# Kernel optimization log

Hardware: AMD Instinct MI355X
Metric: run time of the kernel (lower is better)

Reference implementation:

```python
import jax, jax.numpy as jnp
import numpy as np

N = 100000
E = 3200000
H = 128
ED = 16
P = 6  # 2**(sample_hop+1)-2 with sample_hop=2


def setup_inputs() -> dict:
    key = jax.random.key(0)
    ks = jax.random.split(key, 8)
    q = jax.random.normal(ks[0], (N, H), jnp.float32)
    k = jax.random.normal(ks[1], (N, H), jnp.float32)
    v = jax.random.normal(ks[2], (N, H), jnp.float32)
    eigs = jax.random.normal(ks[3], (N, ED), jnp.float32)
    lambda0 = jnp.zeros((1,), jnp.float32)
    path_emb_w = jax.random.normal(ks[4], (P, 1), jnp.float32)
    indices = jax.random.randint(ks[5], (2, E), 0, N, dtype=jnp.int32)
    path_type = jax.random.randint(ks[6], (E,), 0, P, dtype=jnp.int32)
    return {"q": q, "k": k, "v": v, "eigs": eigs, "lambda0": lambda0,
            "path_emb_w": path_emb_w, "indices": indices, "path_type": path_type}


def _segment_softmax(vals, seg, num_segments):
    # numerically stable softmax over edges grouped by destination row `seg`
    m = jax.ops.segment_max(vals, seg, num_segments=num_segments)
    m = jnp.where(jnp.isfinite(m), m, 0.0)  # empty segments -> 0, harmless
    e = jnp.exp(vals - m[seg])
    d = jax.ops.segment_sum(e, seg, num_segments=num_segments)
    return e / d[seg]


def reference(q, k, v, eigs, lambda0, path_emb_w, indices, path_type):
    row, col = indices[0], indices[1]
    inv_sqrt_dim = 1.0 / jnp.sqrt(jnp.float32(H))
    # per-edge q.k score  [E]
    x = jnp.sum(q[row] * k[col], axis=-1) * inv_sqrt_dim
    # eig bias  [E]
    y = jnp.sum(eigs[row] * eigs[col], axis=-1)
    s0 = x + jnp.exp(lambda0[0]) * y
    # path bias  [E]
    s1 = path_emb_w[path_type, 0]
    a0 = _segment_softmax(s0, row, N)
    a1 = _segment_softmax(s1, row, N)
    s = 0.5 * (a0 + a1)  # stack+mean over the two score channels
    # sparse [N,N] @ v : scatter-add weighted value rows
    out = jax.ops.segment_sum(s[:, None] * v[col], row, num_segments=N)
    return out
```

## Files before the change

### kernel.cpp

```cpp
#include <hip/hip_runtime.h>
#include <math.h>

#define H 128
#define ED 16
#define COLBITS 17
#define COLMASK 0x1FFFF

__device__ __forceinline__ float wsum64(float v) {
#pragma unroll
    for (int o = 32; o > 0; o >>= 1) v += __shfl_xor(v, o, 64);
    return v;
}
__device__ __forceinline__ float wmax64(float v) {
#pragma unroll
    for (int o = 32; o > 0; o >>= 1) v = fmaxf(v, __shfl_xor(v, o, 64));
    return v;
}
__device__ __forceinline__ float bflo(unsigned u) { return __uint_as_float(u << 16); }
__device__ __forceinline__ float bfhi(unsigned u) { return __uint_as_float(u & 0xffff0000u); }
__device__ __forceinline__ unsigned short f2bf(float f) {
    unsigned u = __float_as_uint(f);
    return (unsigned short)((u + 0x7fff + ((u >> 16) & 1)) >> 16);
}

__global__ void k_cast(const float4* __restrict__ src, ushort4* __restrict__ dst, int n4) {
    int i = blockIdx.x * 256 + threadIdx.x;
    if (i >= n4) return;
    float4 f = src[i];
    ushort4 o;
    o.x = f2bf(f.x);
    o.y = f2bf(f.y);
    o.z = f2bf(f.z);
    o.w = f2bf(f.w);
    dst[i] = o;
}

__global__ void k_rank(const int* __restrict__ idx, int* __restrict__ cnt,
                       int* __restrict__ rank, int E) {
    int e = (blockIdx.x * 256 + threadIdx.x) * 4;
    if (e + 3 < E) {
        int4 r = *(const int4*)(idx + e);
        int4 o;
        o.x = atomicAdd(&cnt[r.x], 1);
        o.y = atomicAdd(&cnt[r.y], 1);
        o.z = atomicAdd(&cnt[r.z], 1);
        o.w = atomicAdd(&cnt[r.w], 1);
        *(int4*)(rank + e) = o;
    } else {
        for (; e < E; e++) rank[e] = atomicAdd(&cnt[idx[e]], 1);
    }
}

__global__ void k_scan_blocks(const int* __restrict__ cnt, int* __restrict__ rowstart,
                              int* __restrict__ partials, int n) {
    __shared__ int tmp[256];
    int t = threadIdx.x;
    int i = blockIdx.x * 256 + t;
    int v = (i < n) ? cnt[i] : 0;
    tmp[t] = v;
    __syncthreads();
#pragma unroll
    for (int o = 1; o < 256; o <<= 1) {
        int x = (t >= o) ? tmp[t - o] : 0;
        __syncthreads();
        if (t >= o) tmp[t] += x;
        __syncthreads();
    }
    int incl = tmp[t];
    if (i < n) rowstart[i] = incl - v;
    if (t == 255) partials[blockIdx.x] = incl;
}

__global__ void k_scan_partials(int* __restrict__ partials, int nb) {
    __shared__ int tmp[512];
    int t = threadIdx.x;
    int v = (t < nb) ? partials[t] : 0;
    tmp[t] = v;
    __syncthreads();
#pragma unroll
    for (int o = 1; o < 512; o <<= 1) {
        int x = (t >= o) ? tmp[t - o] : 0;
        __syncthreads();
        if (t >= o) tmp[t] += x;
        __syncthreads();
    }
    if (t < nb) partials[t] = tmp[t] - v;
}

__global__ void k_add_offsets(int* __restrict__ rowstart, const int* __restrict__ partials,
                              int n, int E) {
    int i = blockIdx.x * 256 + threadIdx.x;
    if (i < n) rowstart[i] += partials[blockIdx.x];
    if (i == 0) rowstart[n] = E;
}

__global__ void k_place(const int* __restrict__ idx, const int* __restrict__ ptype,
                        const int* __restrict__ rowstart, const int* __restrict__ rank,
                        int* __restrict__ csr, int E) {
    int e = (blockIdx.x * 256 + threadIdx.x) * 4;
    if (e + 3 < E) {
        int4 r = *(const int4*)(idx + e);
        int4 c = *(const int4*)(idx + E + e);
        int4 p = *(const int4*)(ptype + e);
        int4 rk = *(const int4*)(rank + e);
        csr[rowstart[r.x] + rk.x] = (p.x << COLBITS) | c.x;
        csr[rowstart[r.y] + rk.y] = (p.y << COLBITS) | c.y;
        csr[rowstart[r.z] + rk.z] = (p.z << COLBITS) | c.z;
        csr[rowstart[r.w] + rk.w] = (p.w << COLBITS) | c.w;
    } else {
        for (; e < E; e++)
            csr[rowstart[idx[e]] + rank[e]] = (ptype[e] << COLBITS) | idx[E + e];
    }
}

__global__ __launch_bounds__(256) void k_attn(
    const float* __restrict__ q, const unsigned short* __restrict__ kb,
    const unsigned short* __restrict__ vb, const float* __restrict__ eigs,
    const float* __restrict__ lambda0, const float* __restrict__ pw,
    const int* __restrict__ rowstart, const int* __restrict__ csr,
    float* __restrict__ spill, float* __restrict__ out, int N) {
    const int lane = threadIdx.x & 63;
    const int g = lane >> 4;
    const int s16 = lane & 15;
    const int rowi = blockIdx.x * 4 + (threadIdx.x >> 6);
    if (rowi >= N) return;

    const float el0 = __expf(lambda0[0]);
    const float inv = 0.08838834764831845f;
    const int start = rowstart[rowi];
    const int deg = rowstart[rowi + 1] - start;

    const float4* q4 = (const float4*)q;
    const float4* e4 = (const float4*)eigs;

    if (deg == 0) {
        if (g == 0) {
            float4 z = make_float4(0.f, 0.f, 0.f, 0.f);
            ((float4*)out)[(size_t)rowi * 32 + s16 * 2] = z;
            ((float4*)out)[(size_t)rowi * 32 + s16 * 2 + 1] = z;
        }
        return;
    }

    if (deg <= 128) {
        float s00 = -INFINITY, s01 = -INFINITY, t10 = -INFINITY, t11 = -INFINITY;
        {
            int e0 = 4 * s16 + g;
            if (e0 < deg) t10 = pw[(csr[start + e0] >> COLBITS) & 7];
            int e1 = 64 + 4 * s16 + g;
            if (e1 < deg) t11 = pw[(csr[start + e1] >> COLBITS) & 7];
        }
        float4 qa = q4[(size_t)rowi * 32 + s16 * 2];
        float4 qb = q4[(size_t)rowi * 32 + s16 * 2 + 1];
        float4 ea = make_float4(0.f, 0.f, 0.f, 0.f);
        if (s16 < 4) ea = e4[(size_t)rowi * 4 + s16];

        const int niter = (deg + 3) >> 2;

#pragma unroll 8
        for (int i = 0; i < niter; i++) {
            int rel = 4 * i + g;
            float p = 0.f;
            if (rel < deg) {
                int cm = csr[start + rel] & COLMASK;
                uint4 kr = *(const uint4*)(kb + (size_t)cm * H + s16 * 8);
                p = (qa.x * bflo(kr.x) + qa.y * bfhi(kr.x) + qa.z * bflo(kr.y) +
                     qa.w * bfhi(kr.y) + qb.x * bflo(kr.z) + qb.y * bfhi(kr.z) +
                     qb.z * bflo(kr.w) + qb.w * bfhi(kr.w)) * inv;
                if (s16 < 4) {
                    float4 ev = e4[(size_t)cm * 4 + s16];
                    p += el0 * (ea.x * ev.x + ea.y * ev.y + ea.z * ev.z + ea.w * ev.w);
                }
            }
#pragma unroll
            for (int o = 1; o < 16; o <<= 1) p += __shfl_xor(p, o, 64);
            if (s16 == (i & 15) && rel < deg) {
                if (i < 16) s00 = p;
                else s01 = p;
            }
        }

        float m0 = wmax64(fmaxf(s00, s01));
        float m1 = wmax64(fmaxf(t10, t11));
        float p00 = __expf(s00 - m0), p01 = __expf(s01 - m0);
        float p10 = __expf(t10 - m1), p11 = __expf(t11 - m1);
        float d0 = wsum64(p00 + p01);
        float d1 = wsum64(p10 + p11);
        float r0 = (d0 > 0.f) ? 0.5f / d0 : 0.f;
        float r1 = (d1 > 0.f) ? 0.5f / d1 : 0.f;
        float w0 = p00 * r0 + p10 * r1;
        float w1 = p01 * r0 + p11 * r1;

        float4 acc_a = make_float4(0.f, 0.f, 0.f, 0.f);
        float4 acc_b = make_float4(0.f, 0.f, 0.f, 0.f);
#pragma unroll 8
        for (int i = 0; i < niter; i++) {
            int rel = 4 * i + g;
            int src = (g << 4) | (i & 15);
            float wj = __shfl((i < 16) ? w0 : w1, src, 64);
            if (rel < deg) {
                int cm = csr[start + rel] & COLMASK;
                uint4 vr = *(const uint4*)(vb + (size_t)cm * H + s16 * 8);
                acc_a.x = fmaf(wj, bflo(vr.x), acc_a.x);
                acc_a.y = fmaf(wj, bfhi(vr.x), acc_a.y);
                acc_a.z = fmaf(wj, bflo(vr.y), acc_a.z);
                acc_a.w = fmaf(wj, bfhi(vr.y), acc_a.w);
                acc_b.x = fmaf(wj, bflo(vr.z), acc_b.x);
                acc_b.y = fmaf(wj, bfhi(vr.z), acc_b.y);
                acc_b.z = fmaf(wj, bflo(vr.w), acc_b.z);
                acc_b.w = fmaf(wj, bfhi(vr.w), acc_b.w);
            }
        }
#pragma unroll
        for (int o = 16; o < 64; o <<= 1) {
            acc_a.x += __shfl_xor(acc_a.x, o, 64);
            acc_a.y += __shfl_xor(acc_a.y, o, 64);
            acc_a.z += __shfl_xor(acc_a.z, o, 64);
            acc_a.w += __shfl_xor(acc_a.w, o, 64);
            acc_b.x += __shfl_xor(acc_b.x, o, 64);
            acc_b.y += __shfl_xor(acc_b.y, o, 64);
            acc_b.z += __shfl_xor(acc_b.z, o, 64);
            acc_b.w += __shfl_xor(acc_b.w, o, 64);
        }
        if (g == 0) {
            ((float4*)out)[(size_t)rowi * 32 + s16 * 2] = acc_a;
            ((float4*)out)[(size_t)rowi * 32 + s16 * 2 + 1] = acc_b;
        }
        return;
    }

    const int end = start + deg;
    const float2* q2r = (const float2*)(q + (size_t)rowi * H);
    const float4* erow = (const float4*)(eigs + (size_t)rowi * ED);
    float m0 = -INFINITY, m1 = -INFINITY;
    for (int e0 = start; e0 < end; e0 += 64) {
        int e = e0 + lane;
        float s0f = -INFINITY, s1f = -INFINITY;
        if (e < end) {
            int x = csr[e];
            int cc = x & COLMASK;
            s1f = pw[(x >> COLBITS) & 7];
            const unsigned* kr = (const unsigned*)(kb + (size_t)cc * H);
            float xx = 0.f;
            for (int t = 0; t < H / 2; t++) {
                unsigned u = kr[t];
                float2 qv = q2r[t];
                xx += qv.x * bflo(u) + qv.y * bfhi(u);
            }
            const float4* crow = (const float4*)(eigs + (size_t)cc * ED);
            float yy = 0.f;
#pragma unroll
            for (int t = 0; t < ED / 4; t++) {
                float4 ev = erow[t], cv = crow[t];
                yy += ev.x * cv.x + ev.y * cv.y + ev.z * cv.z + ev.w * cv.w;
            }
            s0f = xx * inv + el0 * yy;
            spill[e] = s0f;
        }
        m0 = fmaxf(m0, s0f);
        m1 = fmaxf(m1, s1f);
    }
    m0 = wmax64(m0);
    m1 = wmax64(m1);
    float d0 = 0.f, d1 = 0.f;
    for (int e0 = start; e0 < end; e0 += 64) {
        int e = e0 + lane;
        if (e < end) {
            int x = csr[e];
            d0 += __expf(spill[e] - m0);
            d1 += __expf(pw[(x >> COLBITS) & 7] - m1);
        }
    }
    d0 = wsum64(d0);
    d1 = wsum64(d1);
    float r0 = (d0 > 0.f) ? 0.5f / d0 : 0.f;
    float r1 = (d1 > 0.f) ? 0.5f / d1 : 0.f;
    float2 acc2 = make_float2(0.f, 0.f);
    for (int e0 = start; e0 < end; e0 += 64) {
        int cnt2 = min(64, end - e0);
        int cc = 0;
        float wv = 0.f;
        if (lane < cnt2) {
            int e = e0 + lane;
            int x = csr[e];
            cc = x & COLMASK;
            wv = __expf(spill[e] - m0) * r0 + __expf(pw[(x >> COLBITS) & 7] - m1) * r1;
        }
        for (int j = 0; j < cnt2; j++) {
            float wj = __shfl(wv, j, 64);
            int cj = __shfl(cc, j, 64);
            unsigned u = ((const unsigned*)(vb))[(size_t)cj * (H / 2) + lane];
            acc2.x = fmaf(wj, bflo(u), acc2.x);
            acc2.y = fmaf(wj, bfhi(u), acc2.y);
        }
    }
    ((float2*)out)[(size_t)rowi * (H / 2) + lane] = acc2;
}

extern "C" void kernel_launch(void* const* d_in, const int* in_sizes, int n_in,
                              void* d_out, int out_size, void* d_ws, size_t ws_size,
                              hipStream_t stream) {
    const float* q = (const float*)d_in[0];
    const float* k = (const float*)d_in[1];
    const float* v = (const float*)d_in[2];
    const float* eigs = (const float*)d_in[3];
    const float* lambda0 = (const float*)d_in[4];
    const float* pw = (const float*)d_in[5];
    const int* indices = (const int*)d_in[6];
    const int* ptype = (const int*)d_in[7];
    float* out = (float*)d_out;

    int N = in_sizes[0] / H;
    int E = in_sizes[6] / 2;

    char* ws = (char*)d_ws;
    int* cnt = (int*)ws;
    int* rowstart = cnt + N;
    int* partials = rowstart + (N + 1);
    size_t off = ((size_t)(N + (N + 1) + 512) * 4 + 15) & ~(size_t)15;
    int* rank = (int*)(ws + off);
    off += (size_t)E * 4;
    int* csr = (int*)(ws + off);
    off += (size_t)E * 4;
    unsigned short* kb = (unsigned short*)(ws + off);
    off += (size_t)N * H * 2;
    unsigned short* vb = (unsigned short*)(ws + off);

    hipMemsetAsync(cnt, 0, (size_t)N * sizeof(int), stream);

    int n4 = N * H / 4;
    int nbC = (n4 + 255) / 256;
    k_cast<<<nbC, 256, 0, stream>>>((const float4*)k, (ushort4*)kb, n4);
    k_cast<<<nbC, 256, 0, stream>>>((const float4*)v, (ushort4*)vb, n4);

    int nbE4 = (E / 4 + 255) / 256;
    int nbN = (N + 255) / 256;
    k_rank<<<nbE4, 256, 0, stream>>>(indices, cnt, rank, E);
    k_scan_blocks<<<nbN, 256, 0, stream>>>(cnt, rowstart, partials, N);
    k_scan_partials<<<1, 512, 0, stream>>>(partials, nbN);
    k_add_offsets<<<nbN, 256, 0, stream>>>(rowstart, partials, N, E);
    k_place<<<nbE4, 256, 0, stream>>>(indices, ptype, rowstart, rank, csr, E);
    k_attn<<<(N + 3) / 4, 256, 0, stream>>>(q, kb, vb, eigs, lambda0, pw, rowstart,
                                            csr, (float*)rank, out, N);
}
```

Measured before the change: 788.4 us.

## Build CSR via two-level bucket sort with LDS histograms instead of global atomics

Replaces the per-row global atomic rank, multi-kernel scan, and scattered placement with a two-pass bucket sort. Edges are grouped into 256-row buckets using shared-memory histograms, staged in contiguous per-bucket regions, then sorted within each bucket by a per-bucket block that also emits rowstart. The two k/v cast kernels are merged into one launch. The aim is to cut contention on global atomics and random scatter traffic. The cost is an extra staging pass and per-bucket work that can be uneven when bucket sizes vary.

New measurement: 660.4 us. 16.2% less time.

```diff
diff --git a/kernel.cpp b/kernel.cpp
--- a/kernel.cpp
+++ b/kernel.cpp
@@ -23,58 +23,68 @@
     return (unsigned short)((u + 0x7fff + ((u >> 16) & 1)) >> 16);
 }
 
-__global__ void k_cast(const float4* __restrict__ src, ushort4* __restrict__ dst, int n4) {
+__global__ __launch_bounds__(256) void k_cast2(const float4* __restrict__ k,
+                                               const float4* __restrict__ v,
+                                               ushort4* __restrict__ kb,
+                                               ushort4* __restrict__ vb, int n4) {
     int i = blockIdx.x * 256 + threadIdx.x;
-    if (i >= n4) return;
-    float4 f = src[i];
+    const float4* src;
+    ushort4* dst;
+    int j;
+    if (i < n4) {
+        src = k; dst = kb; j = i;
+    } else if (i < 2 * n4) {
+        src = v; dst = vb; j = i - n4;
+    } else {
+        return;
+    }
+    float4 f = src[j];
     ushort4 o;
     o.x = f2bf(f.x);
     o.y = f2bf(f.y);
     o.z = f2bf(f.z);
     o.w = f2bf(f.w);
-    dst[i] = o;
-}
-
-__global__ void k_rank(const int* __restrict__ idx, int* __restrict__ cnt,
-                       int* __restrict__ rank, int E) {
-    int e = (blockIdx.x * 256 + threadIdx.x) * 4;
-    if (e + 3 < E) {
-        int4 r = *(const int4*)(idx + e);
-        int4 o;
-        o.x = atomicAdd(&cnt[r.x], 1);
-        o.y = atomicAdd(&cnt[r.y], 1);
-        o.z = atomicAdd(&cnt[r.z], 1);
-        o.w = atomicAdd(&cnt[r.w], 1);
-        *(int4*)(rank + e) = o;
-    } else {
-        for (; e < E; e++) rank[e] = atomicAdd(&cnt[idx[e]], 1);
-    }
-}
-
-__global__ void k_scan_blocks(const int* __restrict__ cnt, int* __restrict__ rowstart,
-                              int* __restrict__ partials, int n) {
-    __shared__ int tmp[256];
+    dst[j] = o;
+}
+
+__global__ __launch_bounds__(256) void k_count(const int* __restrict__ rows,
+                                               int* __restrict__ bcnt, int E, int nb) {
+    __shared__ int h[512];
     int t = threadIdx.x;
-    int i = blockIdx.x * 256 + t;
-    int v = (i < n) ? cnt[i] : 0;
-    tmp[t] = v;
-    __syncthreads();
-#pragma unroll
-    for (int o = 1; o < 256; o <<= 1) {
-        int x = (t >= o) ? tmp[t - o] : 0;
-        __syncthreads();
-        if (t >= o) tmp[t] += x;
-        __syncthreads();
-    }
-    int incl = tmp[t];
-    if (i < n) rowstart[i] = incl - v;
-    if (t == 255) partials[blockIdx.x] = incl;
-}
-
-__global__ void k_scan_partials(int* __restrict__ partials, int nb) {
+    h[t] = 0;
+    h[t + 256] = 0;
+    __syncthreads();
+    int base = blockIdx.x * 4096;
+#pragma unroll
+    for (int j = 0; j < 4; j++) {
+        int e = base + j * 1024 + t * 4;
+        if (e + 3 < E) {
+            int4 r = *(const int4*)(rows + e);
+            atomicAdd(&h[r.x >> 8], 1);
+            atomicAdd(&h[r.y >> 8], 1);
+            atomicAdd(&h[r.z >> 8], 1);
+            atomicAdd(&h[r.w >> 8], 1);
+        } else {
+#pragma unroll
+            for (int q = 0; q < 4; q++) {
+                int e2 = e + q;
+                if (e2 < E) atomicAdd(&h[rows[e2] >> 8], 1);
+            }
+        }
+    }
+    __syncthreads();
+    for (int i = t; i < nb; i += 256) {
+        int c = h[i];
+        if (c) atomicAdd(&bcnt[i], c);
+    }
+}
+
+__global__ void k_scan_bb(const int* __restrict__ bcnt, int* __restrict__ bbase,
+                          int* __restrict__ bcur, int* __restrict__ rowstart, int nb,
+                          int N, int E) {
     __shared__ int tmp[512];
     int t = threadIdx.x;
-    int v = (t < nb) ? partials[t] : 0;
+    int v = (t < nb) ? bcnt[t] : 0;
     tmp[t] = v;
     __syncthreads();
 #pragma unroll
@@ -84,32 +94,115 @@
         if (t >= o) tmp[t] += x;
         __syncthreads();
     }
-    if (t < nb) partials[t] = tmp[t] - v;
-}
-
-__global__ void k_add_offsets(int* __restrict__ rowstart, const int* __restrict__ partials,
-                              int n, int E) {
-    int i = blockIdx.x * 256 + threadIdx.x;
-    if (i < n) rowstart[i] += partials[blockIdx.x];
-    if (i == 0) rowstart[n] = E;
-}
-
-__global__ void k_place(const int* __restrict__ idx, const int* __restrict__ ptype,
-                        const int* __restrict__ rowstart, const int* __restrict__ rank,
-                        int* __restrict__ csr, int E) {
-    int e = (blockIdx.x * 256 + threadIdx.x) * 4;
-    if (e + 3 < E) {
-        int4 r = *(const int4*)(idx + e);
-        int4 c = *(const int4*)(idx + E + e);
-        int4 p = *(const int4*)(ptype + e);
-        int4 rk = *(const int4*)(rank + e);
-        csr[rowstart[r.x] + rk.x] = (p.x << COLBITS) | c.x;
-        csr[rowstart[r.y] + rk.y] = (p.y << COLBITS) | c.y;
-        csr[rowstart[r.z] + rk.z] = (p.z << COLBITS) | c.z;
-        csr[rowstart[r.w] + rk.w] = (p.w << COLBITS) | c.w;
-    } else {
-        for (; e < E; e++)
-            csr[rowstart[idx[e]] + rank[e]] = (ptype[e] << COLBITS) | idx[E + e];
+    if (t < nb) {
+        int ex = tmp[t] - v;
+        bbase[t] = ex;
+        bcur[t] = ex;
+    }
+    if (t == 0) {
+        bbase[nb] = E;
+        rowstart[N] = E;
+    }
+}
+
+__global__ __launch_bounds__(256) void k_bucket(const int* __restrict__ rows,
+                                                const int* __restrict__ cols,
+                                                const int* __restrict__ pts,
+                                                int* __restrict__ bcur,
+                                                int* __restrict__ stage, int E, int nb) {
+    __shared__ int h[512];
+    __shared__ int lbase[512];
+    int t = threadIdx.x;
+    h[t] = 0;
+    h[t + 256] = 0;
+    __syncthreads();
+    int base = blockIdx.x * 4096;
+    int pr[16];
+    int br[16];
+#pragma unroll
+    for (int j = 0; j < 4; j++) {
+        int e = base + j * 1024 + t * 4;
+        if (e + 3 < E) {
+            int4 r = *(const int4*)(rows + e);
+            int4 c = *(const int4*)(cols + e);
+            int4 p = *(const int4*)(pts + e);
+            int k0 = atomicAdd(&h[r.x >> 8], 1);
+            int k1 = atomicAdd(&h[r.y >> 8], 1);
+            int k2 = atomicAdd(&h[r.z >> 8], 1);
+            int k3 = atomicAdd(&h[r.w >> 8], 1);
+            br[j * 4 + 0] = ((r.x >> 8) << 16) | k0;
+            br[j * 4 + 1] = ((r.y >> 8) << 16) | k1;
+            br[j * 4 + 2] = ((r.z >> 8) << 16) | k2;
+            br[j * 4 + 3] = ((r.w >> 8) << 16) | k3;
+            pr[j * 4 + 0] = ((r.x & 255) << 20) | (p.x << COLBITS) | c.x;
+            pr[j * 4 + 1] = ((r.y & 255) << 20) | (p.y << COLBITS) | c.y;
+            pr[j * 4 + 2] = ((r.z & 255) << 20) | (p.z << COLBITS) | c.z;
+            pr[j * 4 + 3] = ((r.w & 255) << 20) | (p.w << COLBITS) | c.w;
+        } else {
+#pragma unroll
+            for (int q = 0; q < 4; q++) {
+                int e2 = e + q;
+                if (e2 < E) {
+                    int r = rows[e2], c = cols[e2], p = pts[e2];
+                    int kk = atomicAdd(&h[r >> 8], 1);
+                    br[j * 4 + q] = ((r >> 8) << 16) | kk;
+                    pr[j * 4 + q] = ((r & 255) << 20) | (p << COLBITS) | c;
+                } else {
+                    br[j * 4 + q] = -1;
+                }
+            }
+        }
+    }
+    __syncthreads();
+    for (int i = t; i < nb; i += 256) {
+        int c = h[i];
+        lbase[i] = c ? atomicAdd(&bcur[i], c) : 0;
+    }
+    __syncthreads();
+#pragma unroll
+    for (int j = 0; j < 16; j++) {
+        int brv = br[j];
+        if (brv >= 0) {
+            int bin = brv >> 16;
+            stage[lbase[bin] + (brv & 0xFFFF)] = pr[j];
+        }
+    }
+}
+
+__global__ __launch_bounds__(256) void k_build(const int* __restrict__ bbase,
+                                               const int* __restrict__ stage,
+                                               int* __restrict__ csr,
+                                               int* __restrict__ rowstart, int N) {
+    __shared__ int h[256];
+    __shared__ int sc[256];
+    __shared__ int cur[256];
+    int b = blockIdx.x;
+    int t = threadIdx.x;
+    int s = bbase[b];
+    int n = bbase[b + 1] - s;
+    h[t] = 0;
+    __syncthreads();
+    for (int i = t; i < n; i += 256) atomicAdd(&h[stage[s + i] >> 20], 1);
+    __syncthreads();
+    int val = h[t];
+    sc[t] = val;
+    __syncthreads();
+#pragma unroll
+    for (int o = 1; o < 256; o <<= 1) {
+        int x = (t >= o) ? sc[t - o] : 0;
+        __syncthreads();
+        if (t >= o) sc[t] += x;
+        __syncthreads();
+    }
+    int excl = sc[t] - val;
+    int row = (b << 8) + t;
+    if (row < N) rowstart[row] = s + excl;
+    cur[t] = excl;
+    __syncthreads();
+    for (int i = t; i < n; i += 256) {
+        int v = stage[s + i];
+        int p = atomicAdd(&cur[v >> 20], 1);
+        csr[s + p] = v & 0xFFFFF;
     }
 }
 
@@ -312,13 +405,15 @@
 
     int N = in_sizes[0] / H;
     int E = in_sizes[6] / 2;
+    int nb = (N + 255) >> 8;
 
     char* ws = (char*)d_ws;
-    int* cnt = (int*)ws;
-    int* rowstart = cnt + N;
-    int* partials = rowstart + (N + 1);
-    size_t off = ((size_t)(N + (N + 1) + 512) * 4 + 15) & ~(size_t)15;
-    int* rank = (int*)(ws + off);
+    int* bcnt = (int*)ws;
+    int* bbase = bcnt + nb;
+    int* bcur = bbase + (nb + 1);
+    int* rowstart = bcur + nb;
+    size_t off = ((size_t)(3 * nb + 1 + N + 1) * 4 + 15) & ~(size_t)15;
+    int* stage = (int*)(ws + off);
     off += (size_t)E * 4;
     int* csr = (int*)(ws + off);
     off += (size_t)E * 4;
@@ -326,20 +421,18 @@
     off += (size_t)N * H * 2;
     unsigned short* vb = (unsigned short*)(ws + off);
 
-    hipMemsetAsync(cnt, 0, (size_t)N * sizeof(int), stream);
+    hipMemsetAsync(bcnt, 0, (size_t)nb * sizeof(int), stream);
 
     int n4 = N * H / 4;
-    int nbC = (n4 + 255) / 256;
-    k_cast<<<nbC, 256, 0, stream>>>((const float4*)k, (ushort4*)kb, n4);
-    k_cast<<<nbC, 256, 0, stream>>>((const float4*)v, (ushort4*)vb, n4);
-
-    int nbE4 = (E / 4 + 255) / 256;
-    int nbN = (N + 255) / 256;
-    k_rank<<<nbE4, 256, 0, stream>>>(indices, cnt, rank, E);
-    k_scan_blocks<<<nbN, 256, 0, stream>>>(cnt, rowstart, partials, N);
-    k_scan_partials<<<1, 512, 0, stream>>>(partials, nbN);
-    k_add_offsets<<<nbN, 256, 0, stream>>>(rowstart, partials, N, E);
-    k_place<<<nbE4, 256, 0, stream>>>(indices, ptype, rowstart, rank, csr, E);
+    int nbC = (2 * n4 + 255) / 256;
+    k_cast2<<<nbC, 256, 0, stream>>>((const float4*)k, (const float4*)v, (ushort4*)kb,
+                                     (ushort4*)vb, n4);
+
+    int nbE = (E + 4095) / 4096;
+    k_count<<<nbE, 256, 0, stream>>>(indices, bcnt, E, nb);
+    k_scan_bb<<<1, 512, 0, stream>>>(bcnt, bbase, bcur, rowstart, nb, N, E);
+    k_bucket<<<nbE, 256, 0, stream>>>(indices, indices + E, ptype, bcur, stage, E, nb);
+    k_build<<<nb, 256, 0, stream>>>(bbase, stage, csr, rowstart, N);
     k_attn<<<(N + 3) / 4, 256, 0, stream>>>(q, kb, vb, eigs, lambda0, pw, rowstart,
-                                            csr, (float*)rank, out, N);
-}
+                                            csr, (float*)stage, out, N);
+}
```
